# Optimization experiments

Hardware: AMD Instinct MI355X
Metric: run time of the kernel (lower is better)

The kernel has to match this reference:

```python
import jax, jax.numpy as jnp
import numpy as np

B, C, H, W = 2, 48, 128, 256
HEADS = 3
EPS_LN = 1e-6
EPS_NRM = 1e-12


def _conv(x, w, b, padding=0, dilation=1, groups=1):
    # x: NCHW, w: OIHW
    out = jax.lax.conv_general_dilated(
        x, w, window_strides=(1, 1),
        padding=[(padding, padding), (padding, padding)],
        rhs_dilation=(dilation, dilation),
        feature_group_count=groups,
        dimension_numbers=('NCHW', 'OIHW', 'NCHW'))
    return out + b[None, :, None, None]


def _ln2d(x, w, b):
    # LayerNorm over channel dim per pixel (NAFNet-style LayerNorm2d)
    mu = x.mean(axis=1, keepdims=True)
    var = ((x - mu) ** 2).mean(axis=1, keepdims=True)
    return (x - mu) / jnp.sqrt(var + EPS_LN) * w[None, :, None, None] + b[None, :, None, None]


def _l2norm(x):
    # F.normalize(dim=-1): x / max(||x||_2, eps)
    n = jnp.sqrt((x * x).sum(-1, keepdims=True))
    return x / jnp.maximum(n, EPS_NRM)


def setup_inputs() -> dict:
    key = jax.random.key(0)
    ks = iter(jax.random.split(key, 40))
    def nrm(shape, s=0.02):
        return jax.random.normal(next(ks), shape, jnp.float32) * s
    d = {
        'x_l': jax.random.normal(next(ks), (B, C, H, W), jnp.float32),
        'x_r': jax.random.normal(next(ks), (B, C, H, W), jnp.float32),
        'ln1_w': jnp.ones((C,), jnp.float32), 'ln1_b': jnp.zeros((C,), jnp.float32),
        'ln2_w': jnp.ones((C,), jnp.float32), 'ln2_b': jnp.zeros((C,), jnp.float32),
        'qkv_l_w': nrm((3 * C, C, 1, 1)), 'qkv_l_b': jnp.zeros((3 * C,), jnp.float32),
        'qkv_r_w': nrm((3 * C, C, 1, 1)), 'qkv_r_b': jnp.zeros((3 * C,), jnp.float32),
        'dw_l_w': nrm((3 * C, 1, 3, 3)), 'dw_l_b': jnp.zeros((3 * C,), jnp.float32),
        'dw_r_w': nrm((3 * C, 1, 3, 3)), 'dw_r_b': jnp.zeros((3 * C,), jnp.float32),
        'dil0_w': nrm((2 * C, 2 * C, 3, 3)), 'dil0_b': jnp.zeros((2 * C,), jnp.float32),
        'dil1_w': nrm((2 * C, 2 * C, 3, 3)), 'dil1_b': jnp.zeros((2 * C,), jnp.float32),
        'dil2_w': nrm((2 * C, 2 * C, 3, 3)), 'dil2_b': jnp.zeros((2 * C,), jnp.float32),
        'convQ_w': nrm((C, 6 * C, 1, 1)), 'convQ_b': jnp.zeros((C,), jnp.float32),
        'conv1_w': nrm((C, C, 1, 1)), 'conv1_b': jnp.zeros((C,), jnp.float32),
        'conv2_w': nrm((C, C, 1, 1)), 'conv2_b': jnp.zeros((C,), jnp.float32),
        'temperature': jnp.ones((HEADS, 1, 1), jnp.float32),
    }
    return d


def reference(x_l, x_r, ln1_w, ln1_b, ln2_w, ln2_b,
              qkv_l_w, qkv_l_b, qkv_r_w, qkv_r_b,
              dw_l_w, dw_l_b, dw_r_w, dw_r_b,
              dil0_w, dil0_b, dil1_w, dil1_b, dil2_w, dil2_b,
              convQ_w, convQ_b, conv1_w, conv1_b, conv2_w, conv2_b,
              temperature):
    b, c, h, w = x_l.shape
    hw = h * w
    ch = c // HEADS  # channels per head

    norm_l = _ln2d(x_l, ln1_w, ln1_b)
    norm_r = _ln2d(x_r, ln2_w, ln2_b)

    qkvl = _conv(_conv(norm_l, qkv_l_w, qkv_l_b), dw_l_w, dw_l_b, padding=1, groups=3 * c)
    qkvr = _conv(_conv(norm_r, qkv_r_w, qkv_r_b), dw_r_w, dw_r_b, padding=1, groups=3 * c)
    Q_l, K_l, V_l = jnp.split(qkvl, 3, axis=1)
    Q_r, K_r, V_r = jnp.split(qkvr, 3, axis=1)

    Q = jnp.concatenate((Q_l, Q_r), axis=1)  # [b, 2c, h, w]
    Q = jnp.concatenate((
        _conv(Q, dil0_w, dil0_b, padding=2, dilation=2),
        _conv(Q, dil1_w, dil1_b, padding=4, dilation=4),
        _conv(Q, dil2_w, dil2_b, padding=6, dilation=6)), axis=1)  # [b, 6c, h, w]
    Q = _conv(Q, convQ_w, convQ_b)  # [b, c, h, w]

    def heads(t):
        return t.reshape(b, HEADS, ch, hw)

    Q = _l2norm(heads(Q))
    K_l = _l2norm(heads(K_l))
    K_r = _l2norm(heads(K_r))
    V_l = heads(V_l)
    V_r = heads(V_r)

    # channel attention: [b, head, ch, ch]
    A_r2l = jax.nn.softmax(jnp.einsum('bhcn,bhdn->bhcd', Q, K_r) * temperature, axis=-1)
    A_l2r = jax.nn.softmax(jnp.einsum('bhcn,bhdn->bhcd', Q, K_l) * temperature, axis=-1)

    F_l = jnp.einsum('bhcd,bhdn->bhcn', A_r2l, V_l).reshape(b, c, h, w)
    F_r = jnp.einsum('bhcd,bhdn->bhcn', A_l2r, V_r).reshape(b, c, h, w)

    F_l = _conv(F_l, conv1_w, conv1_b)
    F_r = _conv(F_r, conv2_w, conv2_b)
    return (x_l + F_l, x_r + F_r)
```

## Files before the change

kernel.cpp:

```cpp
#include <hip/hip_runtime.h>
#include <hip/hip_bf16.h>

typedef __hip_bfloat16 bf16;
typedef __attribute__((ext_vector_type(8))) short short8;
typedef __attribute__((ext_vector_type(4))) float f32x4;
typedef unsigned int u32;

constexpr int IMG_H = 128;
constexpr int IMG_W = 256;
constexpr int HW    = IMG_H * IMG_W;
constexpr int BB    = 2;
constexpr int CC    = 48;
constexpr int C3    = 144;
constexpr int XPW   = 268;
constexpr int XOFF  = 6;

constexpr int WO_QKVL_W = 0;
constexpr int WO_QKVR_W = 6912;
constexpr int WO_DWL_W  = 13824;
constexpr int WO_DWR_W  = 15120;
constexpr int WO_C1_W   = 16416;
constexpr int WO_C2_W   = 18720;
constexpr int WO_QKVL_B = 21024;
constexpr int WO_QKVR_B = 21168;
constexpr int WO_DWL_B  = 21312;
constexpr int WO_DWR_B  = 21456;
constexpr int WO_C1_B   = 21600;
constexpr int WO_C2_B   = 21648;
constexpr int WO_LN1W   = 21696;
constexpr int WO_LN1B   = 21744;
constexpr int WO_LN2W   = 21792;
constexpr int WO_LN2B   = 21840;
constexpr int WO_TEMP   = 21888;
constexpr int WO_WQ     = 21952;
constexpr int WO_D0W    = 35776;
constexpr int WO_D1W    = 118720;
constexpr int WO_D2W    = 201664;
constexpr int WO_BQ     = 284608;
constexpr int WO_B0     = 284656;
constexpr int WO_B1     = 284752;
constexpr int WO_B2     = 284848;
constexpr int WO_WPACK  = 284944;
constexpr int WO_EFFB   = 409360;
constexpr int WO_NQ     = 409424;
constexpr int WO_NKL    = 409520;
constexpr int WO_NKR    = 409616;
constexpr int WO_AR2L   = 409712;
constexpr int WO_AL2R   = 411248;
constexpr int WO_M1     = 412800;
constexpr int WO_M2     = 417408;
constexpr int WO_WQP    = 422016;
constexpr int WO_PART   = 431232;

constexpr size_t ACT_BASE_BYTES = 2118144;

constexpr size_t A_P  = 0;
constexpr size_t A_Q1 = 9437184;
constexpr size_t A_Q2 = 18874368;
constexpr size_t A_QC = 28311552;

struct PrepArgs {
  const void* src[25];
  int dst[25];
  int n[25];
};

__device__ __forceinline__ bool probe_bf16(const void* ln1w) {
  return ((const unsigned short*)ln1w)[0] == 0x3F80;
}

__global__ __launch_bounds__(256) void prep_k(PrepArgs a, float* __restrict__ wsf) {
  bool isb = probe_bf16(a.src[12]);
  int t = blockIdx.y;
  int i = blockIdx.x * 256 + threadIdx.x;
  if (i < a.n[t]) {
    float v = isb ? __bfloat162float(((const bf16*)a.src[t])[i])
                  : ((const float*)a.src[t])[i];
    wsf[a.dst[t] + i] = v;
  }
}

__global__ __launch_bounds__(512) void effw2_k(const float* __restrict__ wsf,
                                               bf16* __restrict__ wpack) {
  int d  = blockIdx.x / 96;
  int ci = blockIdx.x % 96;
  __shared__ float wds[864];
  __shared__ float wqs[48 * 97];
  const int wdb = (d == 0) ? WO_D0W : (d == 1) ? WO_D1W : WO_D2W;
  for (int idx = threadIdx.x; idx < 864; idx += 512) {
    int m = idx / 9, tt = idx % 9;
    wds[idx] = wsf[wdb + (m * 96 + ci) * 9 + tt];
  }
  for (int idx = threadIdx.x; idx < 4608; idx += 512) {
    int co = idx / 96, m = idx % 96;
    wqs[co * 97 + m] = wsf[WO_WQ + co * 288 + d * 96 + m];
  }
  __syncthreads();
  int tco = threadIdx.x;
  if (tco < 432) {
    int t = tco / 48, co = tco % 48;
    float s = 0.f;
#pragma unroll 8
    for (int m = 0; m < 96; ++m) s += wqs[co * 97 + m] * wds[m * 9 + t];
    int trow = t / 3, dxi = t % 3;
    int ti = (trow == 0) ? (2 - d) * 3 + dxi
           : (trow == 1) ? 9 + d * 3 + dxi
                         : 18 + d * 3 + dxi;
    int kc = ci >> 5, j = ci & 7;
    int L = ((ci & 31) >> 3) * 16 + (co & 15);
    int nt = co >> 4;
    int f = (ti * 3 + kc) * 3 + nt;
    wpack[(size_t)f * 512 + L * 8 + j] = __float2bfloat16(s);
  }
}

__global__ __launch_bounds__(64) void effb_k(const float* __restrict__ wsf,
                                             float* __restrict__ effb) {
  int co = threadIdx.x;
  if (co >= 48) return;
  float s = wsf[WO_BQ + co];
  for (int m = 0; m < 96; ++m) {
    s += wsf[WO_WQ + co * 288 + m]       * wsf[WO_B0 + m];
    s += wsf[WO_WQ + co * 288 + 96 + m]  * wsf[WO_B1 + m];
    s += wsf[WO_WQ + co * 288 + 192 + m] * wsf[WO_B2 + m];
  }
  effb[co] = s;
}

__global__ __launch_bounds__(256) void wqp_k(const float* __restrict__ wsf,
                                             bf16* __restrict__ wqp) {
  int idx = blockIdx.x * 256 + threadIdx.x;
  if (idx >= 18432) return;
  int side = idx / 9216;
  int rem = idx % 9216;
  int nt = rem / 1024;
  int kt = (rem / 512) % 2;
  int e  = rem % 512;
  int L = e >> 3, j = e & 7;
  int o = nt * 16 + (L & 15);
  int kp = kt * 32 + (L >> 4) * 8 + j;
  int g = kp >> 4, r = kp & 15;
  float val = 0.f;
  if (r < 12) {
    int c = g * 12 + r;
    val = wsf[(side ? WO_QKVR_W : WO_QKVL_W) + o * 48 + c];
  }
  wqp[idx] = __float2bfloat16(val);
}

__global__ __launch_bounds__(256) void lnqkv_k(
    const void* __restrict__ x, const void* __restrict__ probe,
    const float* __restrict__ lnw, const float* __restrict__ lnb,
    const bf16* __restrict__ wqp_side, const float* __restrict__ qb,
    bf16* __restrict__ pre) {
  __shared__ __align__(16) unsigned char LDSU[21504 + 18432];
  bf16* XNs = (bf16*)LDSU;
  float2* red = (float2*)(LDSU + 9216);
  bf16* Cs = (bf16*)LDSU;
  bf16* W = (bf16*)(LDSU + 21504);
  int tid = threadIdx.x;
  for (int i = tid; i < 1152; i += 256)
    ((uint4*)W)[i] = ((const uint4*)wqp_side)[i];

  int px = tid & 63;
  int w = tid >> 6;
  int p = blockIdx.x * 64 + px;
  int b = p >> 15;
  int pix = p & (HW - 1);
  size_t base = (size_t)b * CC * HW + pix;
  float v[12];
  if (probe_bf16(probe)) {
    const bf16* xp = (const bf16*)x + base;
#pragma unroll
    for (int c = 0; c < 12; ++c)
      v[c] = __bfloat162float(xp[(size_t)(w * 12 + c) * HW]);
  } else {
    const float* xp = (const float*)x + base;
#pragma unroll
    for (int c = 0; c < 12; ++c) v[c] = xp[(size_t)(w * 12 + c) * HW];
  }
  float s = 0.f, s2 = 0.f;
#pragma unroll
  for (int c = 0; c < 12; ++c) { s += v[c]; s2 += v[c] * v[c]; }
  red[w * 64 + px] = make_float2(s, s2);
  __syncthreads();
  float S = 0.f, S2 = 0.f;
#pragma unroll
  for (int i = 0; i < 4; ++i) {
    float2 r2 = red[i * 64 + px];
    S += r2.x; S2 += r2.y;
  }
  float mu = S * (1.f / 48.f);
  float var = S2 * (1.f / 48.f) - mu * mu;
  float rs = rsqrtf(var + 1e-6f);
  bf16 o16[16];
#pragma unroll
  for (int c = 0; c < 12; ++c)
    o16[c] = __float2bfloat16((v[c] - mu) * rs * lnw[w * 12 + c] + lnb[w * 12 + c]);
#pragma unroll
  for (int c = 12; c < 16; ++c) o16[c] = __float2bfloat16(0.f);
  *(uint4*)(XNs + px * 72 + w * 16) = *(uint4*)(o16);
  *(uint4*)(XNs + px * 72 + w * 16 + 8) = *(uint4*)(o16 + 8);
  __syncthreads();

  int L = tid & 63;
  int lo = L & 15, hi = L >> 4;
  const bf16* arow = XNs + (size_t)(w * 16 + lo) * 72 + hi * 8;
  short8 a0 = *(const short8*)(arow);
  short8 a1 = *(const short8*)(arow + 32);
  __syncthreads();
#pragma unroll
  for (int nt = 0; nt < 9; ++nt) {
    float bvv = qb[nt * 16 + lo];
    f32x4 acc = {bvv, bvv, bvv, bvv};
    acc = __builtin_amdgcn_mfma_f32_16x16x32_bf16(
        a0, *(const short8*)(W + (nt * 2 + 0) * 512 + L * 8), acc, 0, 0, 0);
    acc = __builtin_amdgcn_mfma_f32_16x16x32_bf16(
        a1, *(const short8*)(W + (nt * 2 + 1) * 512 + L * 8), acc, 0, 0, 0);
#pragma unroll
    for (int r = 0; r < 4; ++r)
      Cs[(nt * 16 + lo) * 66 + w * 16 + hi * 4 + r] = __float2bfloat16(acc[r]);
  }
  __syncthreads();
  int pix0 = (blockIdx.x * 64) & (HW - 1);
#pragma unroll
  for (int pass = 0; pass < 18; ++pass) {
    int o = pass * 8 + (tid >> 5);
    int px2 = (tid & 31) * 2;
    bf16 t2[2];
    t2[0] = Cs[o * 66 + px2];
    t2[1] = Cs[o * 66 + px2 + 1];
    *(unsigned*)(pre + ((size_t)(b * C3 + o)) * HW + pix0 + px2) = *(unsigned*)t2;
  }
}

__global__ __launch_bounds__(256) void dw_k(
    const bf16* __restrict__ in, const float* __restrict__ w9,
    const float* __restrict__ bias, bf16* __restrict__ out) {
  int gid = blockIdx.x;
  int yt = gid & 15;
  int c = (gid >> 4) % C3;
  int b = gid / (16 * C3);
  int ry = threadIdx.x >> 5, xi = threadIdx.x & 31;
  int y = yt * 8 + ry;
  int x0 = xi * 8;
  const bf16* base = in + ((size_t)(b * C3 + c)) * HW;
  float wv[9];
#pragma unroll
  for (int t = 0; t < 9; ++t) wv[t] = w9[c * 9 + t];
  float bz = bias[c];
  float acc[8];
#pragma unroll
  for (int i = 0; i < 8; ++i) acc[i] = bz;
#pragma unroll
  for (int ky = 0; ky < 3; ++ky) {
    int yy = y + ky - 1;
    if ((unsigned)yy >= (unsigned)IMG_H) continue;
    const bf16* row = base + yy * IMG_W + x0;
    uint4 m = *(const uint4*)(row);
    float f[10];
    f[0] = (x0 > 0) ? __bfloat162float(row[-1]) : 0.f;
    f[9] = (x0 + 8 < IMG_W) ? __bfloat162float(row[8]) : 0.f;
    f[1] = __uint_as_float(m.x << 16);
    f[2] = __uint_as_float(m.x & 0xFFFF0000u);
    f[3] = __uint_as_float(m.y << 16);
    f[4] = __uint_as_float(m.y & 0xFFFF0000u);
    f[5] = __uint_as_float(m.z << 16);
    f[6] = __uint_as_float(m.z & 0xFFFF0000u);
    f[7] = __uint_as_float(m.w << 16);
    f[8] = __uint_as_float(m.w & 0xFFFF0000u);
    float w0 = wv[ky * 3], w1 = wv[ky * 3 + 1], w2 = wv[ky * 3 + 2];
#pragma unroll
    for (int i = 0; i < 8; ++i)
      acc[i] += w0 * f[i] + w1 * f[i + 1] + w2 * f[i + 2];
  }
  bf16 o[8];
#pragma unroll
  for (int i = 0; i < 8; ++i) o[i] = __float2bfloat16(acc[i]);
  *(uint4*)(out + ((size_t)(b * C3 + c)) * HW + y * IMG_W + x0) = *(uint4*)o;
}

__global__ __launch_bounds__(256) void qc_k(const bf16* __restrict__ q1,
                                            const bf16* __restrict__ q2,
                                            bf16* __restrict__ qc) {
  int b = blockIdx.x >> 7;
  int y = blockIdx.x & 127;
  int half = blockIdx.y;
  int tid = threadIdx.x;
  int x0 = half * 128;
  int px = tid & 127;
  int cig = tid >> 7;
  __shared__ __align__(16) bf16 T[128][100];
#pragma unroll 8
  for (int k = 0; k < 48; ++k) {
    int ci = cig * 48 + k;
    const bf16* src = (ci < 48)
        ? q1 + (((size_t)(b * C3 + ci)) * IMG_H + y) * IMG_W
        : q2 + (((size_t)(b * C3 + ci - 48)) * IMG_H + y) * IMG_W;
    T[px][ci] = src[x0 + px];
  }
  __syncthreads();
  size_t rowbase = ((size_t)(b * IMG_H + y)) * XPW * 96 + (size_t)half * 12864;
#pragma unroll 1
  for (int i = 0; i < 13; ++i) {
    int e4 = i * 256 + tid;
    if (e4 >= 3216) break;
    int e = e4 * 4;
    int xp = (e + half * 12864) / 96;
    int ci = (e + half * 12864) % 96;
    int x = xp - XOFF;
    uint2 val;
    if ((unsigned)x < (unsigned)IMG_W) {
      val = *(const uint2*)(&T[x - x0][ci]);
    } else {
      val.x = 0u; val.y = 0u;
    }
    *(uint2*)(qc + rowbase + e) = val;
  }
}

__global__ __launch_bounds__(256, 1) void dil_mfma_k(
    const bf16* __restrict__ qc, const bf16* __restrict__ wp,
    const float* __restrict__ effb, bf16* __restrict__ qh) {
  __shared__ __align__(16) unsigned char LDSU[51456];
  bf16* Arow = (bf16*)LDSU;
  float* Cs  = (float*)LDSU;

  int bid = blockIdx.x;
  int xcd = bid & 7;
  int slot = bid >> 3;
  int y = xcd * 16 + (slot & 15);
  int b = slot >> 4;
  int tid = threadIdx.x;
  int L = tid & 63;
  int w = tid >> 6;
  int lo = L & 15, hi = L >> 4;

  f32x4 acc[4][3];
#pragma unroll
  for (int g2 = 0; g2 < 4; ++g2)
#pragma unroll
    for (int nt = 0; nt < 3; ++nt) {
      float bv = effb[nt * 16 + lo];
      acc[g2][nt] = {bv, bv, bv, bv};
    }

  const bf16* wrow = wp + L * 8;
  short8 wc[9];
#pragma unroll
  for (int f = 0; f < 9; ++f)
    wc[f] = *(const short8*)(wrow + f * 512);

  int dy_prev = -100;
#pragma unroll 1
  for (int g = 0; g < 9; ++g) {
    int D = (g < 3) ? (6 - 2 * g) : (g < 6) ? (2 * (g - 2)) : (2 * (g - 5));
    int dy = (g < 3) ? -D : (g < 6) ? 0 : D;
    int yy = y + dy;
    bool valid = (unsigned)yy < (unsigned)IMG_H;
    if (valid && dy != dy_prev) {
      __syncthreads();
      const bf16* src = qc + (size_t)(b * IMG_H + yy) * (XPW * 96);
#pragma unroll
      for (int r = 0; r < 13; ++r) {
        int c = w + r * 4;
        if (c < 51) {
          int i = c * 64 + L;
          if (i < 3216) {
            __builtin_amdgcn_global_load_lds(
                (const __attribute__((address_space(1))) u32*)(src + (size_t)i * 8),
                (__attribute__((address_space(3))) u32*)(Arow + (size_t)c * 512),
                16, 0, 0);
          }
        }
      }
      __syncthreads();
      dy_prev = dy;
    }
#pragma unroll
    for (int dxi = 0; dxi < 3; ++dxi) {
      int ti = g * 3 + dxi;
      short8 wn[9];
      if (ti < 26) {
        const bf16* wr = wrow + (ti + 1) * 4608;
#pragma unroll
        for (int f = 0; f < 9; ++f)
          wn[f] = *(const short8*)(wr + f * 512);
      }
      if (valid) {
        int dx = (dxi - 1) * D;
        const bf16* ar = Arow + (size_t)(XOFF + dx + w * 64 + lo) * 96 + hi * 8;
#pragma unroll
        for (int g2 = 0; g2 < 4; ++g2)
#pragma unroll
          for (int kc = 0; kc < 3; ++kc) {
            short8 a = *(const short8*)(ar + g2 * (16 * 96) + kc * 32);
#pragma unroll
            for (int nt = 0; nt < 3; ++nt)
              acc[g2][nt] = __builtin_amdgcn_mfma_f32_16x16x32_bf16(
                  a, wc[kc * 3 + nt], acc[g2][nt], 0, 0, 0);
          }
      }
      if (ti < 26) {
#pragma unroll
        for (int f = 0; f < 9; ++f) wc[f] = wn[f];
      }
    }
  }

  __syncthreads();
#pragma unroll
  for (int g2 = 0; g2 < 4; ++g2)
#pragma unroll
    for (int nt = 0; nt < 3; ++nt)
#pragma unroll
      for (int r = 0; r < 4; ++r)
        Cs[(nt * 16 + lo) * 260 + w * 64 + g2 * 16 + hi * 4 + r] = acc[g2][nt][r];
  __syncthreads();
  size_t obase = (size_t)b * CC * HW + (size_t)y * IMG_W;
#pragma unroll 1
  for (int i = 0; i < 12; ++i) {
    int chunk = i * 256 + tid;
    int co = chunk >> 6;
    int px4 = (chunk & 63) * 4;
    const float* s = Cs + co * 260 + px4;
    bf16 t4[4];
    t4[0] = __float2bfloat16(s[0]);
    t4[1] = __float2bfloat16(s[1]);
    t4[2] = __float2bfloat16(s[2]);
    t4[3] = __float2bfloat16(s[3]);
    *(uint2*)(qh + obase + (size_t)co * HW + px4) = *(uint2*)t4;
  }
}

__device__ __forceinline__ float wave_sum(float v) {
#pragma unroll
  for (int off = 32; off > 0; off >>= 1) v += __shfl_down(v, off, 64);
  return v;
}

__device__ __forceinline__ float blo(unsigned u) {
  return __uint_as_float(u << 16);
}
__device__ __forceinline__ float bhi(unsigned u) {
  return __uint_as_float(u & 0xFFFF0000u);
}

__global__ __launch_bounds__(256) void rownorm_k(
    const bf16* __restrict__ qh, const bf16* __restrict__ qkvl,
    const bf16* __restrict__ qkvr, float* __restrict__ nq,
    float* __restrict__ nkl, float* __restrict__ nkr) {
  int id = blockIdx.x;
  int which = id / 96;
  int rid = id % 96;
  int b = rid / 48;
  int c = rid % 48;
  const bf16* ptr = (which == 0) ? qh + ((size_t)(b * CC + c)) * HW
                  : (which == 1) ? qkvl + ((size_t)(b * C3 + 48 + c)) * HW
                                 : qkvr + ((size_t)(b * C3 + 48 + c)) * HW;
  float s = 0.f;
#pragma unroll 2
  for (int it = 0; it < 16; ++it) {
    int n0 = (it * 256 + threadIdx.x) * 8;
    uint4 u = *(const uint4*)(ptr + n0);
    float a0 = blo(u.x), a1 = bhi(u.x), a2 = blo(u.y), a3 = bhi(u.y);
    float a4 = blo(u.z), a5 = bhi(u.z), a6 = blo(u.w), a7 = bhi(u.w);
    s += a0 * a0 + a1 * a1 + a2 * a2 + a3 * a3 + a4 * a4 + a5 * a5 +
         a6 * a6 + a7 * a7;
  }
  s = wave_sum(s);
  __shared__ float red[4];
  if ((threadIdx.x & 63) == 0) red[threadIdx.x >> 6] = s;
  __syncthreads();
  if (threadIdx.x == 0) {
    float tot = red[0] + red[1] + red[2] + red[3];
    float* dst = (which == 0) ? nq : (which == 1) ? nkl : nkr;
    dst[rid] = tot;
  }
}

__global__ __launch_bounds__(256) void logits_mfma_k(
    const bf16* __restrict__ qh, const bf16* __restrict__ qkvl,
    const bf16* __restrict__ qkvr, float* __restrict__ part) {
  int abh = blockIdx.x;
  int chunk = blockIdx.y;
  int a = abh / 6;
  int b = (abh / 3) % 2;
  int h = abh % 3;
  int tid = threadIdx.x;
  int L = tid & 63, w = tid >> 6;
  int lo = L & 15, hi = L >> 4;
  const bf16* qrow = qh + ((size_t)(b * CC + h * 16 + lo)) * HW;
  const bf16* krow =
      ((a == 0) ? qkvr : qkvl) + ((size_t)(b * C3 + 48 + h * 16 + lo)) * HW;
  int px0 = chunk * 1024 + w * 256 + hi * 8;
  f32x4 acc = {0.f, 0.f, 0.f, 0.f};
#pragma unroll
  for (int s = 0; s < 8; ++s) {
    short8 av = *(const short8*)(qrow + px0 + s * 32);
    short8 bv = *(const short8*)(krow + px0 + s * 32);
    acc = __builtin_amdgcn_mfma_f32_16x16x32_bf16(av, bv, acc, 0, 0, 0);
  }
  __shared__ float red[4][256];
#pragma unroll
  for (int r = 0; r < 4; ++r) red[w][(hi * 4 + r) * 16 + lo] = acc[r];
  __syncthreads();
  float sum = red[0][tid] + red[1][tid] + red[2][tid] + red[3][tid];
  part[((size_t)abh * 32 + chunk) * 256 + tid] = sum;
}

__global__ __launch_bounds__(256) void logits_red_k(
    const float* __restrict__ part, const float* __restrict__ nq,
    const float* __restrict__ nkl, const float* __restrict__ nkr,
    const float* __restrict__ temp, float* __restrict__ logr2l,
    float* __restrict__ logl2r) {
  int abh = blockIdx.x;
  int a = abh / 6, b = (abh / 3) % 2, h = abh % 3;
  int t = threadIdx.x;
  int i = t >> 4, j = t & 15;
  float s = 0.f;
  const float* p = part + (size_t)abh * 32 * 256 + t;
#pragma unroll 8
  for (int c = 0; c < 32; ++c) s += p[c * 256];
  float qn = fmaxf(sqrtf(nq[b * 48 + h * 16 + i]), 1e-12f);
  float kn = fmaxf(sqrtf(((a == 0) ? nkr : nkl)[b * 48 + h * 16 + j]), 1e-12f);
  float val = s / (qn * kn) * temp[h];
  ((a == 0) ? logr2l : logl2r)[b * 768 + h * 256 + i * 16 + j] = val;
}

__global__ __launch_bounds__(256) void softmaxM_k(float* __restrict__ wsf) {
  int tid = threadIdx.x;
  __shared__ float A1[1536], A2[1536];
  if (tid < 192) {
    const float* p = wsf + ((tid < 96) ? WO_AR2L : WO_AL2R) + (tid % 96) * 16;
    float* dst = ((tid < 96) ? A1 : A2) + (tid % 96) * 16;
    float m = -1e30f;
#pragma unroll
    for (int j = 0; j < 16; ++j) m = fmaxf(m, p[j]);
    float s = 0.f;
    float e[16];
#pragma unroll
    for (int j = 0; j < 16; ++j) {
      e[j] = expf(p[j] - m);
      s += e[j];
    }
    float inv = 1.f / s;
#pragma unroll
    for (int j = 0; j < 16; ++j) dst[j] = e[j] * inv;
  }
  __syncthreads();
#pragma unroll 1
  for (int idx = tid; idx < 4608; idx += 256) {
    int b = idx / 2304;
    int r = idx % 2304;
    int o = r / 48;
    int cp = r % 48;
    int h = cp >> 4, j = cp & 15;
    const float* a1 = &A1[((b * 3 + h) * 16) * 16 + j];
    const float* a2 = &A2[((b * 3 + h) * 16) * 16 + j];
    float s1 = 0.f, s2 = 0.f;
#pragma unroll
    for (int i = 0; i < 16; ++i) {
      s1 += wsf[WO_C1_W + o * 48 + h * 16 + i] * a1[i * 16];
      s2 += wsf[WO_C2_W + o * 48 + h * 16 + i] * a2[i * 16];
    }
    wsf[WO_M1 + idx] = s1;
    wsf[WO_M2 + idx] = s2;
  }
}

__global__ __launch_bounds__(256) void attn_out2_k(
    const bf16* __restrict__ q1, const bf16* __restrict__ q2,
    const void* __restrict__ x1, const void* __restrict__ x2,
    const void* __restrict__ probe, const float* __restrict__ Mall,
    const float* __restrict__ cball, void* __restrict__ out) {
  int side = blockIdx.z;
  const bf16* qkv = side ? q2 : q1;
  const void* x = side ? x2 : x1;
  const float* M = Mall + side * 4608;
  const float* cb = cball + side * 48;
  int tid = threadIdx.x;
  int p = blockIdx.x * 256 + tid;
  int b = __builtin_amdgcn_readfirstlane(p >> 15);
  int pix = p & (HW - 1);
  int o0 = blockIdx.y * 16;
  bool isb = probe_bf16(probe);

  float v[CC];
  const bf16* vb = qkv + ((size_t)(b * C3 + 96)) * HW + pix;
#pragma unroll
  for (int c = 0; c < CC; ++c) v[c] = __bfloat162float(vb[(size_t)c * HW]);

  const float* Mb = M + b * 2304;
  size_t base = (size_t)b * CC * HW + pix;
  float res[16];
#pragma unroll 2
  for (int o = 0; o < 16; ++o) {
    float acc = cb[o0 + o];
    const float* mrow = Mb + (o0 + o) * 48;
#pragma unroll
    for (int c = 0; c < CC; ++c) acc += mrow[c] * v[c];
    res[o] = acc;
  }
  size_t obase = (size_t)side * BB * CC * HW + base + (size_t)o0 * HW;
  if (isb) {
    const bf16* xp = (const bf16*)x + base + (size_t)o0 * HW;
    bf16* op = (bf16*)out + obase;
#pragma unroll
    for (int o = 0; o < 16; ++o)
      op[(size_t)o * HW] =
          __float2bfloat16(res[o] + __bfloat162float(xp[(size_t)o * HW]));
  } else {
    const float* xp = (const float*)x + base + (size_t)o0 * HW;
    float* op = (float*)out + obase;
#pragma unroll
    for (int o = 0; o < 16; ++o) op[(size_t)o * HW] = res[o] + xp[(size_t)o * HW];
  }
}

extern "C" void kernel_launch(void* const* d_in, const int* in_sizes, int n_in,
                              void* d_out, int out_size, void* d_ws, size_t ws_size,
                              hipStream_t stream) {
  (void)in_sizes; (void)n_in; (void)out_size; (void)ws_size;
  const void* x_l = d_in[0];
  const void* x_r = d_in[1];
  const void* probe = d_in[2];
  float* wsf = (float*)d_ws;
  bf16* wpack = (bf16*)(wsf + WO_WPACK);
  bf16* wqp = (bf16*)(wsf + WO_WQP);
  bf16* act = (bf16*)((char*)d_ws + ACT_BASE_BYTES);
  bf16* P  = act + A_P;
  bf16* Q1 = act + A_Q1;
  bf16* Q2 = act + A_Q2;
  bf16* QC = act + A_QC;
  bf16* qh = P;

  PrepArgs pa;
  const int srcIdx[25] = {6, 8, 10, 12, 22, 24, 7, 9, 11, 13, 23, 25,
                          2, 3, 4, 5, 26, 20, 14, 16, 18, 21, 15, 17, 19};
  const int dstOff[25] = {WO_QKVL_W, WO_QKVR_W, WO_DWL_W, WO_DWR_W, WO_C1_W, WO_C2_W,
                          WO_QKVL_B, WO_QKVR_B, WO_DWL_B, WO_DWR_B, WO_C1_B, WO_C2_B,
                          WO_LN1W, WO_LN1B, WO_LN2W, WO_LN2B, WO_TEMP,
                          WO_WQ, WO_D0W, WO_D1W, WO_D2W, WO_BQ, WO_B0, WO_B1, WO_B2};
  const int ns[25] = {6912, 6912, 1296, 1296, 2304, 2304, 144, 144, 144, 144,
                      48, 48, 48, 48, 48, 48, 3,
                      13824, 82944, 82944, 82944, 48, 96, 96, 96};
  for (int i = 0; i < 25; ++i) {
    pa.src[i] = d_in[srcIdx[i]];
    pa.dst[i] = dstOff[i];
    pa.n[i] = ns[i];
  }
  prep_k<<<dim3(324, 25), 256, 0, stream>>>(pa, wsf);

  effw2_k<<<288, 512, 0, stream>>>(wsf, wpack);
  effb_k<<<1, 64, 0, stream>>>(wsf, wsf + WO_EFFB);
  wqp_k<<<72, 256, 0, stream>>>(wsf, wqp);

  lnqkv_k<<<1024, 256, 0, stream>>>(x_l, probe, wsf + WO_LN1W, wsf + WO_LN1B,
                                    wqp, wsf + WO_QKVL_B, P);
  dw_k<<<BB * C3 * 16, 256, 0, stream>>>(P, wsf + WO_DWL_W, wsf + WO_DWL_B, Q1);
  lnqkv_k<<<1024, 256, 0, stream>>>(x_r, probe, wsf + WO_LN2W, wsf + WO_LN2B,
                                    wqp + 9216, wsf + WO_QKVR_B, P);
  dw_k<<<BB * C3 * 16, 256, 0, stream>>>(P, wsf + WO_DWR_W, wsf + WO_DWR_B, Q2);

  qc_k<<<dim3(BB * IMG_H, 2), 256, 0, stream>>>(Q1, Q2, QC);

  dil_mfma_k<<<256, 256, 0, stream>>>(QC, wpack, wsf + WO_EFFB, qh);

  rownorm_k<<<288, 256, 0, stream>>>(qh, Q1, Q2, wsf + WO_NQ,
                                     wsf + WO_NKL, wsf + WO_NKR);
  logits_mfma_k<<<dim3(12, 32), 256, 0, stream>>>(qh, Q1, Q2, wsf + WO_PART);
  logits_red_k<<<12, 256, 0, stream>>>(wsf + WO_PART, wsf + WO_NQ,
                                       wsf + WO_NKL, wsf + WO_NKR,
                                       wsf + WO_TEMP, wsf + WO_AR2L,
                                       wsf + WO_AL2R);
  softmaxM_k<<<1, 256, 0, stream>>>(wsf);

  attn_out2_k<<<dim3(256, 3, 2), 256, 0, stream>>>(
      Q1, Q2, x_l, x_r, probe, wsf + WO_M1, wsf + WO_C1_B, d_out);
}
```

Measured before the change: 275.0 us.

## Fuse row norms into logits kernel, pad QC rows, merge small kernels

```diff
diff --git a/kernel.cpp b/kernel.cpp
--- a/kernel.cpp
+++ b/kernel.cpp
@@ -14,6 +14,10 @@
 constexpr int C3    = 144;
 constexpr int XPW   = 268;
 constexpr int XOFF  = 6;
+constexpr int QCP   = 104;
+constexpr int QCS   = XPW * QCP;
+constexpr int QCH   = QCS / 2;
+constexpr int QCCH  = QCS / 8;
 
 constexpr int WO_QKVL_W = 0;
 constexpr int WO_QKVR_W = 6912;
@@ -42,15 +46,13 @@
 constexpr int WO_B2     = 284848;
 constexpr int WO_WPACK  = 284944;
 constexpr int WO_EFFB   = 409360;
-constexpr int WO_NQ     = 409424;
-constexpr int WO_NKL    = 409520;
-constexpr int WO_NKR    = 409616;
 constexpr int WO_AR2L   = 409712;
 constexpr int WO_AL2R   = 411248;
 constexpr int WO_M1     = 412800;
 constexpr int WO_M2     = 417408;
 constexpr int WO_WQP    = 422016;
 constexpr int WO_PART   = 431232;
+constexpr int WO_PART2  = WO_D0W;
 
 constexpr size_t ACT_BASE_BYTES = 2118144;
 
@@ -114,21 +116,22 @@
   }
 }
 
-__global__ __launch_bounds__(64) void effb_k(const float* __restrict__ wsf,
+__global__ __launch_bounds__(256) void wqp_k(const float* __restrict__ wsf,
+                                             bf16* __restrict__ wqp,
                                              float* __restrict__ effb) {
-  int co = threadIdx.x;
-  if (co >= 48) return;
-  float s = wsf[WO_BQ + co];
-  for (int m = 0; m < 96; ++m) {
-    s += wsf[WO_WQ + co * 288 + m]       * wsf[WO_B0 + m];
-    s += wsf[WO_WQ + co * 288 + 96 + m]  * wsf[WO_B1 + m];
-    s += wsf[WO_WQ + co * 288 + 192 + m] * wsf[WO_B2 + m];
-  }
-  effb[co] = s;
-}
-
-__global__ __launch_bounds__(256) void wqp_k(const float* __restrict__ wsf,
-                                             bf16* __restrict__ wqp) {
+  if (blockIdx.x == 72) {
+    int co = threadIdx.x;
+    if (co < 48) {
+      float s = wsf[WO_BQ + co];
+      for (int m = 0; m < 96; ++m) {
+        s += wsf[WO_WQ + co * 288 + m]       * wsf[WO_B0 + m];
+        s += wsf[WO_WQ + co * 288 + 96 + m]  * wsf[WO_B1 + m];
+        s += wsf[WO_WQ + co * 288 + 192 + m] * wsf[WO_B2 + m];
+      }
+      effb[co] = s;
+    }
+    return;
+  }
   int idx = blockIdx.x * 256 + threadIdx.x;
   if (idx >= 18432) return;
   int side = idx / 9216;
@@ -300,20 +303,19 @@
     T[px][ci] = src[x0 + px];
   }
   __syncthreads();
-  size_t rowbase = ((size_t)(b * IMG_H + y)) * XPW * 96 + (size_t)half * 12864;
+  size_t rowbase = ((size_t)(b * IMG_H + y)) * QCS;
 #pragma unroll 1
-  for (int i = 0; i < 13; ++i) {
+  for (int i = 0; i < 14; ++i) {
     int e4 = i * 256 + tid;
-    if (e4 >= 3216) break;
-    int e = e4 * 4;
-    int xp = (e + half * 12864) / 96;
-    int ci = (e + half * 12864) % 96;
+    if (e4 >= QCH / 4) break;
+    int e = e4 * 4 + half * QCH;
+    int xp = e / QCP;
+    int cin = e % QCP;
     int x = xp - XOFF;
     uint2 val;
-    if ((unsigned)x < (unsigned)IMG_W) {
-      val = *(const uint2*)(&T[x - x0][ci]);
-    } else {
-      val.x = 0u; val.y = 0u;
+    val.x = 0u; val.y = 0u;
+    if ((unsigned)x < (unsigned)IMG_W && cin < 96) {
+      val = *(const uint2*)(&T[x - x0][cin]);
     }
     *(uint2*)(qc + rowbase + e) = val;
   }
@@ -322,7 +324,7 @@
 __global__ __launch_bounds__(256, 1) void dil_mfma_k(
     const bf16* __restrict__ qc, const bf16* __restrict__ wp,
     const float* __restrict__ effb, bf16* __restrict__ qh) {
-  __shared__ __align__(16) unsigned char LDSU[51456];
+  __shared__ __align__(16) unsigned char LDSU[55744];
   bf16* Arow = (bf16*)LDSU;
   float* Cs  = (float*)LDSU;
 
@@ -360,18 +362,16 @@
     bool valid = (unsigned)yy < (unsigned)IMG_H;
     if (valid && dy != dy_prev) {
       __syncthreads();
-      const bf16* src = qc + (size_t)(b * IMG_H + yy) * (XPW * 96);
-#pragma unroll
-      for (int r = 0; r < 13; ++r) {
+      const bf16* src = qc + (size_t)(b * IMG_H + yy) * QCS;
+#pragma unroll
+      for (int r = 0; r < 14; ++r) {
         int c = w + r * 4;
-        if (c < 51) {
-          int i = c * 64 + L;
-          if (i < 3216) {
-            __builtin_amdgcn_global_load_lds(
-                (const __attribute__((address_space(1))) u32*)(src + (size_t)i * 8),
-                (__attribute__((address_space(3))) u32*)(Arow + (size_t)c * 512),
-                16, 0, 0);
-          }
+        int i = c * 64 + L;
+        if (i < QCCH) {
+          __builtin_amdgcn_global_load_lds(
+              (const __attribute__((address_space(1))) u32*)(src + (size_t)i * 8),
+              (__attribute__((address_space(3))) u32*)(Arow + (size_t)c * 512),
+              16, 0, 0);
         }
       }
       __syncthreads();
@@ -389,12 +389,12 @@
       }
       if (valid) {
         int dx = (dxi - 1) * D;
-        const bf16* ar = Arow + (size_t)(XOFF + dx + w * 64 + lo) * 96 + hi * 8;
+        const bf16* ar = Arow + (size_t)(XOFF + dx + w * 64 + lo) * QCP + hi * 8;
 #pragma unroll
         for (int g2 = 0; g2 < 4; ++g2)
 #pragma unroll
           for (int kc = 0; kc < 3; ++kc) {
-            short8 a = *(const short8*)(ar + g2 * (16 * 96) + kc * 32);
+            short8 a = *(const short8*)(ar + g2 * (16 * QCP) + kc * 32);
 #pragma unroll
             for (int nt = 0; nt < 3; ++nt)
               acc[g2][nt] = __builtin_amdgcn_mfma_f32_16x16x32_bf16(
@@ -433,12 +433,6 @@
   }
 }
 
-__device__ __forceinline__ float wave_sum(float v) {
-#pragma unroll
-  for (int off = 32; off > 0; off >>= 1) v += __shfl_down(v, off, 64);
-  return v;
-}
-
 __device__ __forceinline__ float blo(unsigned u) {
   return __uint_as_float(u << 16);
 }
@@ -446,42 +440,10 @@
   return __uint_as_float(u & 0xFFFF0000u);
 }
 
-__global__ __launch_bounds__(256) void rownorm_k(
-    const bf16* __restrict__ qh, const bf16* __restrict__ qkvl,
-    const bf16* __restrict__ qkvr, float* __restrict__ nq,
-    float* __restrict__ nkl, float* __restrict__ nkr) {
-  int id = blockIdx.x;
-  int which = id / 96;
-  int rid = id % 96;
-  int b = rid / 48;
-  int c = rid % 48;
-  const bf16* ptr = (which == 0) ? qh + ((size_t)(b * CC + c)) * HW
-                  : (which == 1) ? qkvl + ((size_t)(b * C3 + 48 + c)) * HW
-                                 : qkvr + ((size_t)(b * C3 + 48 + c)) * HW;
-  float s = 0.f;
-#pragma unroll 2
-  for (int it = 0; it < 16; ++it) {
-    int n0 = (it * 256 + threadIdx.x) * 8;
-    uint4 u = *(const uint4*)(ptr + n0);
-    float a0 = blo(u.x), a1 = bhi(u.x), a2 = blo(u.y), a3 = bhi(u.y);
-    float a4 = blo(u.z), a5 = bhi(u.z), a6 = blo(u.w), a7 = bhi(u.w);
-    s += a0 * a0 + a1 * a1 + a2 * a2 + a3 * a3 + a4 * a4 + a5 * a5 +
-         a6 * a6 + a7 * a7;
-  }
-  s = wave_sum(s);
-  __shared__ float red[4];
-  if ((threadIdx.x & 63) == 0) red[threadIdx.x >> 6] = s;
-  __syncthreads();
-  if (threadIdx.x == 0) {
-    float tot = red[0] + red[1] + red[2] + red[3];
-    float* dst = (which == 0) ? nq : (which == 1) ? nkl : nkr;
-    dst[rid] = tot;
-  }
-}
-
 __global__ __launch_bounds__(256) void logits_mfma_k(
     const bf16* __restrict__ qh, const bf16* __restrict__ qkvl,
-    const bf16* __restrict__ qkvr, float* __restrict__ part) {
+    const bf16* __restrict__ qkvr, float* __restrict__ part,
+    float* __restrict__ part2) {
   int abh = blockIdx.x;
   int chunk = blockIdx.y;
   int a = abh / 6;
@@ -495,37 +457,67 @@
       ((a == 0) ? qkvr : qkvl) + ((size_t)(b * C3 + 48 + h * 16 + lo)) * HW;
   int px0 = chunk * 1024 + w * 256 + hi * 8;
   f32x4 acc = {0.f, 0.f, 0.f, 0.f};
+  float aq = 0.f, ak = 0.f;
 #pragma unroll
   for (int s = 0; s < 8; ++s) {
     short8 av = *(const short8*)(qrow + px0 + s * 32);
     short8 bv = *(const short8*)(krow + px0 + s * 32);
     acc = __builtin_amdgcn_mfma_f32_16x16x32_bf16(av, bv, acc, 0, 0, 0);
+#pragma unroll
+    for (int j = 0; j < 4; ++j) {
+      u32 ua = ((const u32*)&av)[j];
+      u32 ub = ((const u32*)&bv)[j];
+      float q0 = blo(ua), q1 = bhi(ua);
+      float k0 = blo(ub), k1 = bhi(ub);
+      aq += q0 * q0 + q1 * q1;
+      ak += k0 * k0 + k1 * k1;
+    }
   }
   __shared__ float red[4][256];
+  __shared__ float sq[256], sk[256];
 #pragma unroll
   for (int r = 0; r < 4; ++r) red[w][(hi * 4 + r) * 16 + lo] = acc[r];
+  sq[tid] = aq;
+  sk[tid] = ak;
   __syncthreads();
   float sum = red[0][tid] + red[1][tid] + red[2][tid] + red[3][tid];
   part[((size_t)abh * 32 + chunk) * 256 + tid] = sum;
+  if (tid < 32) {
+    const float* srcr = (tid < 16) ? sq : sk;
+    int lo2 = tid & 15;
+    float s = 0.f;
+#pragma unroll
+    for (int w2 = 0; w2 < 4; ++w2)
+#pragma unroll
+      for (int h2 = 0; h2 < 4; ++h2) s += srcr[w2 * 64 + h2 * 16 + lo2];
+    part2[((size_t)abh * 32 + chunk) * 32 + tid] = s;
+  }
 }
 
 __global__ __launch_bounds__(256) void logits_red_k(
-    const float* __restrict__ part, const float* __restrict__ nq,
-    const float* __restrict__ nkl, const float* __restrict__ nkr,
+    const float* __restrict__ part, const float* __restrict__ part2,
     const float* __restrict__ temp, float* __restrict__ logr2l,
     float* __restrict__ logl2r) {
   int abh = blockIdx.x;
-  int a = abh / 6, b = (abh / 3) % 2, h = abh % 3;
+  int a = abh / 6, h = abh % 3;
+  int bnum = (abh / 3) % 2;
   int t = threadIdx.x;
   int i = t >> 4, j = t & 15;
+  __shared__ float nrm[32];
+  if (t < 32) {
+    float s = 0.f;
+    const float* p2 = part2 + (size_t)abh * 32 * 32 + t;
+#pragma unroll 8
+    for (int c = 0; c < 32; ++c) s += p2[c * 32];
+    nrm[t] = fmaxf(sqrtf(s), 1e-12f);
+  }
   float s = 0.f;
   const float* p = part + (size_t)abh * 32 * 256 + t;
 #pragma unroll 8
   for (int c = 0; c < 32; ++c) s += p[c * 256];
-  float qn = fmaxf(sqrtf(nq[b * 48 + h * 16 + i]), 1e-12f);
-  float kn = fmaxf(sqrtf(((a == 0) ? nkr : nkl)[b * 48 + h * 16 + j]), 1e-12f);
-  float val = s / (qn * kn) * temp[h];
-  ((a == 0) ? logr2l : logl2r)[b * 768 + h * 256 + i * 16 + j] = val;
+  __syncthreads();
+  float val = s / (nrm[i] * nrm[16 + j]) * temp[h];
+  ((a == 0) ? logr2l : logl2r)[bnum * 768 + h * 256 + i * 16 + j] = val;
 }
 
 __global__ __launch_bounds__(256) void softmaxM_k(float* __restrict__ wsf) {
@@ -574,7 +566,7 @@
     const void* __restrict__ x1, const void* __restrict__ x2,
     const void* __restrict__ probe, const float* __restrict__ Mall,
     const float* __restrict__ cball, void* __restrict__ out) {
-  int side = blockIdx.z;
+  int side = blockIdx.y;
   const bf16* qkv = side ? q2 : q1;
   const void* x = side ? x2 : x1;
   const float* M = Mall + side * 4608;
@@ -583,7 +575,6 @@
   int p = blockIdx.x * 256 + tid;
   int b = __builtin_amdgcn_readfirstlane(p >> 15);
   int pix = p & (HW - 1);
-  int o0 = blockIdx.y * 16;
   bool isb = probe_bf16(probe);
 
   float v[CC];
@@ -593,28 +584,30 @@
 
   const float* Mb = M + b * 2304;
   size_t base = (size_t)b * CC * HW + pix;
-  float res[16];
-#pragma unroll 2
-  for (int o = 0; o < 16; ++o) {
-    float acc = cb[o0 + o];
-    const float* mrow = Mb + (o0 + o) * 48;
-#pragma unroll
-    for (int c = 0; c < CC; ++c) acc += mrow[c] * v[c];
-    res[o] = acc;
-  }
-  size_t obase = (size_t)side * BB * CC * HW + base + (size_t)o0 * HW;
+  size_t obase = (size_t)side * BB * CC * HW + base;
   if (isb) {
-    const bf16* xp = (const bf16*)x + base + (size_t)o0 * HW;
+    const bf16* xp = (const bf16*)x + base;
     bf16* op = (bf16*)out + obase;
-#pragma unroll
-    for (int o = 0; o < 16; ++o)
+#pragma unroll 4
+    for (int o = 0; o < CC; ++o) {
+      float acc = cb[o];
+      const float* mrow = Mb + o * 48;
+#pragma unroll
+      for (int c = 0; c < CC; ++c) acc += mrow[c] * v[c];
       op[(size_t)o * HW] =
-          __float2bfloat16(res[o] + __bfloat162float(xp[(size_t)o * HW]));
+          __float2bfloat16(acc + __bfloat162float(xp[(size_t)o * HW]));
+    }
   } else {
-    const float* xp = (const float*)x + base + (size_t)o0 * HW;
+    const float* xp = (const float*)x + base;
     float* op = (float*)out + obase;
-#pragma unroll
-    for (int o = 0; o < 16; ++o) op[(size_t)o * HW] = res[o] + xp[(size_t)o * HW];
+#pragma unroll 4
+    for (int o = 0; o < CC; ++o) {
+      float acc = cb[o];
+      const float* mrow = Mb + o * 48;
+#pragma unroll
+      for (int c = 0; c < CC; ++c) acc += mrow[c] * v[c];
+      op[(size_t)o * HW] = acc + xp[(size_t)o * HW];
+    }
   }
 }
 
@@ -653,8 +646,7 @@
   prep_k<<<dim3(324, 25), 256, 0, stream>>>(pa, wsf);
 
   effw2_k<<<288, 512, 0, stream>>>(wsf, wpack);
-  effb_k<<<1, 64, 0, stream>>>(wsf, wsf + WO_EFFB);
-  wqp_k<<<72, 256, 0, stream>>>(wsf, wqp);
+  wqp_k<<<73, 256, 0, stream>>>(wsf, wqp, wsf + WO_EFFB);
 
   lnqkv_k<<<1024, 256, 0, stream>>>(x_l, probe, wsf + WO_LN1W, wsf + WO_LN1B,
                                     wqp, wsf + WO_QKVL_B, P);
@@ -667,15 +659,13 @@
 
   dil_mfma_k<<<256, 256, 0, stream>>>(QC, wpack, wsf + WO_EFFB, qh);
 
-  rownorm_k<<<288, 256, 0, stream>>>(qh, Q1, Q2, wsf + WO_NQ,
-                                     wsf + WO_NKL, wsf + WO_NKR);
-  logits_mfma_k<<<dim3(12, 32), 256, 0, stream>>>(qh, Q1, Q2, wsf + WO_PART);
-  logits_red_k<<<12, 256, 0, stream>>>(wsf + WO_PART, wsf + WO_NQ,
-                                       wsf + WO_NKL, wsf + WO_NKR,
+  logits_mfma_k<<<dim3(12, 32), 256, 0, stream>>>(qh, Q1, Q2, wsf + WO_PART,
+                                                  wsf + WO_PART2);
+  logits_red_k<<<12, 256, 0, stream>>>(wsf + WO_PART, wsf + WO_PART2,
                                        wsf + WO_TEMP, wsf + WO_AR2L,
                                        wsf + WO_AL2R);
   softmaxM_k<<<1, 256, 0, stream>>>(wsf);
 
-  attn_out2_k<<<dim3(256, 3, 2), 256, 0, stream>>>(
+  attn_out2_k<<<dim3(256, 2), 256, 0, stream>>>(
       Q1, Q2, x_l, x_r, probe, wsf + WO_M1, wsf + WO_C1_B, d_out);
 }
```

Result: no change. 276.6 us (+0.6%).
